# Kernel tuning notes

Hardware: AMD Instinct MI355X
Metric: run time of the kernel (lower is better)

Reference implementation:

```python
import jax, jax.numpy as jnp
import numpy as np

DIM = 2048
NUM_HEADS = 16
HEAD_DIM = DIM // NUM_HEADS
ROPE_BASE = 10000.0


def _rope_cos_sin(seq_len, head_dim, dtype):
    # lucidrains-style interleaved rotary embedding
    inv_freq = 1.0 / (ROPE_BASE ** (jnp.arange(0, head_dim, 2, dtype=jnp.float32) / head_dim))
    t = jnp.arange(seq_len, dtype=jnp.float32)
    freqs = t[:, None] * inv_freq[None, :]            # [n, d/2]
    freqs = jnp.repeat(freqs, 2, axis=-1)             # [n, d] interleaved repeat
    return jnp.cos(freqs).astype(dtype), jnp.sin(freqs).astype(dtype)


def _rotate_half(x):
    # interleaved pairs: (x1, x2) -> (-x2, x1)
    x = x.reshape(x.shape[:-1] + (x.shape[-1] // 2, 2))
    x1, x2 = x[..., 0], x[..., 1]
    return jnp.stack((-x2, x1), axis=-1).reshape(x.shape[:-2] + (-1,))


def _apply_rope(x, cos, sin):
    # x: [b, h, n, d]; cos/sin: [n, d]
    return x * cos + _rotate_half(x) * sin


def setup_inputs() -> dict:
    key = jax.random.key(0)
    ks = jax.random.split(key, 9)
    s = 1.0 / np.sqrt(DIM)
    x = jax.random.normal(ks[0], (2, 2048, DIM), dtype=jnp.float32)
    Wq = jax.random.normal(ks[1], (DIM, DIM), dtype=jnp.float32) * s
    Wk = jax.random.normal(ks[2], (DIM, DIM), dtype=jnp.float32) * s
    Wv = jax.random.normal(ks[3], (DIM, DIM), dtype=jnp.float32) * s
    Wo = jax.random.normal(ks[4], (DIM, DIM), dtype=jnp.float32) * s
    bq = jax.random.normal(ks[5], (DIM,), dtype=jnp.float32) * 0.01
    bk = jax.random.normal(ks[6], (DIM,), dtype=jnp.float32) * 0.01
    bv = jax.random.normal(ks[7], (DIM,), dtype=jnp.float32) * 0.01
    bo = jax.random.normal(ks[8], (DIM,), dtype=jnp.float32) * 0.01
    return {"x": x, "Wq": Wq, "bq": bq, "Wk": Wk, "bk": bk,
            "Wv": Wv, "bv": bv, "Wo": Wo, "bo": bo}


def reference(x, Wq, bq, Wk, bk, Wv, bv, Wo, bo):
    b, n, _ = x.shape
    h, d = NUM_HEADS, HEAD_DIM
    # Q/K/V projections; weights stored as [in, out]
    q = (x @ Wq + bq).reshape(b, n, h, d).transpose(0, 2, 1, 3)  # [b,h,n,d]
    k = (x @ Wk + bk).reshape(b, n, h, d).transpose(0, 2, 1, 3)
    v = (x @ Wv + bv).reshape(b, n, h, d).transpose(0, 2, 1, 3)
    cos, sin = _rope_cos_sin(n, d, x.dtype)
    q = _apply_rope(q, cos, sin)
    k = _apply_rope(k, cos, sin)
    # module divides q by sqrt(d), then SDPA applies its own 1/sqrt(d)
    scale = 1.0 / jnp.sqrt(jnp.asarray(d, dtype=x.dtype))
    q = q * scale
    logits = jnp.einsum('bhqd,bhkd->bhqk', q, k) * scale
    attn = jax.nn.softmax(logits, axis=-1)
    out = jnp.einsum('bhqk,bhkd->bhqd', attn, v)          # [b,h,n,d]
    out = out.transpose(0, 2, 1, 3).reshape(b, n, h * d)  # [b,n,dim]
    return out @ Wo + bo
```

## Files before the change

kernel.cpp:

```cpp
#include <hip/hip_runtime.h>
#include <hip/hip_bf16.h>
#include <math.h>

typedef unsigned short u16;
typedef unsigned int u32;
typedef __attribute__((ext_vector_type(8))) short short8;
typedef __attribute__((ext_vector_type(4))) float f32x4;

typedef const __attribute__((address_space(1))) u32 gu32;
typedef __attribute__((address_space(3))) u32 lu32;

#define DIM 2048
#define SEQ 2048
#define NH 16
#define HD 128

static __device__ __forceinline__ u16 f2b(float f) {
  __hip_bfloat16 h = __float2bfloat16(f);
  return __builtin_bit_cast(u16, h);
}
static __device__ __forceinline__ float b2f(u16 u) {
  __hip_bfloat16 h = __builtin_bit_cast(__hip_bfloat16, u);
  return __bfloat162float(h);
}

static __device__ __forceinline__ void g2l16(const u16* g, u16* l) {
  __builtin_amdgcn_global_load_lds((gu32*)g, (lu32*)l, 16, 0, 0);
}

__global__ __launch_bounds__(256) void prep_kernel(const float* __restrict__ x,
                                                   const float* __restrict__ Wq,
                                                   const float* __restrict__ Wk,
                                                   const float* __restrict__ Wv,
                                                   const float* __restrict__ Wo,
                                                   u16* __restrict__ xb,
                                                   u16* __restrict__ WT,
                                                   float* __restrict__ tab) {
  __shared__ float tile[64][65];
  int bid = blockIdx.x;
  int t = threadIdx.x;
  if (bid < 4096) {
    size_t i = ((size_t)bid * 256 + t) * 8;
    float4 a = *(const float4*)(x + i);
    float4 b = *(const float4*)(x + i + 4);
    uint4 o;
    o.x = (u32)f2b(a.x) | ((u32)f2b(a.y) << 16);
    o.y = (u32)f2b(a.z) | ((u32)f2b(a.w) << 16);
    o.z = (u32)f2b(b.x) | ((u32)f2b(b.y) << 16);
    o.w = (u32)f2b(b.z) | ((u32)f2b(b.w) << 16);
    *(uint4*)(xb + i) = o;
  } else if (bid < 8192) {
    int b2 = bid - 4096;
    int z = b2 >> 10;
    int rem = b2 & 1023;
    int by = rem >> 5, bx = rem & 31;
    const float* W = (z == 0) ? Wq : (z == 1) ? Wk : (z == 2) ? Wv : Wo;
    u16* dst = WT + (size_t)z * DIM * DIM;
    int k0 = by * 64, n0 = bx * 64;
    int c = (t & 15) * 4;
    int r = t >> 4;
#pragma unroll
    for (int i = 0; i < 4; ++i) {
      float4 v = *(const float4*)(W + (size_t)(k0 + r + 16 * i) * DIM + n0 + c);
      tile[r + 16 * i][c + 0] = v.x;
      tile[r + 16 * i][c + 1] = v.y;
      tile[r + 16 * i][c + 2] = v.z;
      tile[r + 16 * i][c + 3] = v.w;
    }
    __syncthreads();
#pragma unroll
    for (int i = 0; i < 4; ++i) {
      int rn = r + 16 * i;
      uint2 o;
      o.x = (u32)f2b(tile[c + 0][rn]) | ((u32)f2b(tile[c + 1][rn]) << 16);
      o.y = (u32)f2b(tile[c + 2][rn]) | ((u32)f2b(tile[c + 3][rn]) << 16);
      *(uint2*)(dst + (size_t)(n0 + rn) * DIM + k0 + c) = o;
    }
  } else {
    int idx = (bid - 8192) * 256 + t;
    int n = idx >> 6, j = idx & 63;
    double ang = (double)n * pow(10000.0, -(double)j / 64.0);
    tab[2 * idx + 0] = (float)cos(ang);
    tab[2 * idx + 1] = (float)sin(ang);
  }
}

__global__ __launch_bounds__(256, 2) void qkv_gemm_kernel(const u16* __restrict__ A,
                                                          const u16* __restrict__ Bt,
                                                          const float* __restrict__ bq,
                                                          const float* __restrict__ bk,
                                                          const float* __restrict__ bv,
                                                          const float* __restrict__ tab,
                                                          u16* __restrict__ Qbuf,
                                                          u16* __restrict__ Kbuf,
                                                          u16* __restrict__ Vtbf) {
  __shared__ u16 Asub[2][128 * 64];
  __shared__ u16 Bsub[2][128 * 64];
  int t = threadIdx.x;
  int lane = t & 63, wid = t >> 6;
  int L15 = lane & 15, quad = lane >> 4;
  int wm = (wid >> 1) * 64, wn = (wid & 1) * 64;
  int m0 = blockIdx.y * 128, n0 = blockIdx.x * 128;
  int srow = lane >> 3, schunk = lane & 7;

  f32x4 acc[4][4];
#pragma unroll
  for (int mi = 0; mi < 4; ++mi)
#pragma unroll
    for (int ni = 0; ni < 4; ++ni)
#pragma unroll
      for (int r = 0; r < 4; ++r) acc[mi][ni][r] = 0.f;

  auto stage = [&](int buf, int k0) {
#pragma unroll
    for (int i = 0; i < 4; ++i) {
      int ra = wid * 32 + i * 8 + srow;
      int cs = schunk ^ (ra & 7);
      g2l16(A + (size_t)(m0 + ra) * DIM + k0 + cs * 8, &Asub[buf][(wid * 32 + i * 8) * 64]);
      g2l16(Bt + (size_t)(n0 + ra) * DIM + k0 + cs * 8, &Bsub[buf][(wid * 32 + i * 8) * 64]);
    }
  };

  stage(0, 0);
  for (int it = 0; it < DIM / 64; ++it) {
    __syncthreads();
    if (it + 1 < DIM / 64) stage((it + 1) & 1, (it + 1) * 64);
    int buf = it & 1;
#pragma unroll
    for (int kc = 0; kc < 2; ++kc) {
      short8 af[4], bfr[4];
#pragma unroll
      for (int mi = 0; mi < 4; ++mi) {
        int row = wm + mi * 16 + L15;
        af[mi] = *(const short8*)(&Asub[buf][row * 64 + (((kc * 4 + quad) ^ (L15 & 7)) * 8)]);
      }
#pragma unroll
      for (int ni = 0; ni < 4; ++ni) {
        int row = wn + ni * 16 + L15;
        bfr[ni] = *(const short8*)(&Bsub[buf][row * 64 + (((kc * 4 + quad) ^ (L15 & 7)) * 8)]);
      }
#pragma unroll
      for (int mi = 0; mi < 4; ++mi)
#pragma unroll
        for (int ni = 0; ni < 4; ++ni)
          acc[mi][ni] = __builtin_amdgcn_mfma_f32_16x16x32_bf16(af[mi], bfr[ni], acc[mi][ni], 0, 0, 0);
    }
  }

  int which = n0 >> 11;
  const float* bp = (which == 0) ? bq : (which == 1) ? bk : bv;
#pragma unroll
  for (int mi = 0; mi < 4; ++mi) {
#pragma unroll
    for (int ni = 0; ni < 4; ++ni) {
      int colg = n0 + wn + ni * 16 + L15;
      int col = colg & 2047;
      float bvv = bp[col];
      int h = col >> 7, d = col & 127;
#pragma unroll
      for (int r = 0; r < 4; ++r) {
        int row = m0 + wm + mi * 16 + quad * 4 + r;
        int b = row >> 11, nseq = row & 2047;
        float v = acc[mi][ni][r] + bvv;
        if (which < 2) {
          int j = d >> 1;
          float2 cs = ((const float2*)tab)[nseq * 64 + j];
          float p = __shfl_xor(v, 1, 64);
          float o = (d & 1) ? (v * cs.x + p * cs.y) : (v * cs.x - p * cs.y);
          if (which == 0) o *= (1.0f / 128.0f);
          u16* dst = (which == 0) ? Qbuf : Kbuf;
          dst[((size_t)(b * 16 + h) * SEQ + nseq) * HD + d] = f2b(o);
        } else {
          Vtbf[((size_t)(b * 16 + h) * HD + d) * SEQ + nseq] = f2b(v);
        }
      }
    }
  }
}

__global__ __launch_bounds__(256, 2) void o_gemm_kernel(const u16* __restrict__ A,
                                                        const u16* __restrict__ Bt,
                                                        const float* __restrict__ bias,
                                                        float* __restrict__ Cout) {
  __shared__ u16 Asub[2][128 * 64];
  __shared__ u16 Bsub[2][128 * 64];
  int t = threadIdx.x;
  int lane = t & 63, wid = t >> 6;
  int L15 = lane & 15, quad = lane >> 4;
  int wm = (wid >> 1) * 64, wn = (wid & 1) * 64;
  int m0 = blockIdx.y * 128, n0 = blockIdx.x * 128;
  int srow = lane >> 3, schunk = lane & 7;

  f32x4 acc[4][4];
#pragma unroll
  for (int mi = 0; mi < 4; ++mi)
#pragma unroll
    for (int ni = 0; ni < 4; ++ni)
#pragma unroll
      for (int r = 0; r < 4; ++r) acc[mi][ni][r] = 0.f;

  auto stage = [&](int buf, int k0) {
#pragma unroll
    for (int i = 0; i < 4; ++i) {
      int ra = wid * 32 + i * 8 + srow;
      int cs = schunk ^ (ra & 7);
      g2l16(A + (size_t)(m0 + ra) * DIM + k0 + cs * 8, &Asub[buf][(wid * 32 + i * 8) * 64]);
      g2l16(Bt + (size_t)(n0 + ra) * DIM + k0 + cs * 8, &Bsub[buf][(wid * 32 + i * 8) * 64]);
    }
  };

  stage(0, 0);
  for (int it = 0; it < DIM / 64; ++it) {
    __syncthreads();
    if (it + 1 < DIM / 64) stage((it + 1) & 1, (it + 1) * 64);
    int buf = it & 1;
#pragma unroll
    for (int kc = 0; kc < 2; ++kc) {
      short8 af[4], bfr[4];
#pragma unroll
      for (int mi = 0; mi < 4; ++mi) {
        int row = wm + mi * 16 + L15;
        af[mi] = *(const short8*)(&Asub[buf][row * 64 + (((kc * 4 + quad) ^ (L15 & 7)) * 8)]);
      }
#pragma unroll
      for (int ni = 0; ni < 4; ++ni) {
        int row = wn + ni * 16 + L15;
        bfr[ni] = *(const short8*)(&Bsub[buf][row * 64 + (((kc * 4 + quad) ^ (L15 & 7)) * 8)]);
      }
#pragma unroll
      for (int mi = 0; mi < 4; ++mi)
#pragma unroll
        for (int ni = 0; ni < 4; ++ni)
          acc[mi][ni] = __builtin_amdgcn_mfma_f32_16x16x32_bf16(af[mi], bfr[ni], acc[mi][ni], 0, 0, 0);
    }
  }

#pragma unroll
  for (int mi = 0; mi < 4; ++mi) {
#pragma unroll
    for (int ni = 0; ni < 4; ++ni) {
      int col = n0 + wn + ni * 16 + L15;
      float bvv = bias[col];
#pragma unroll
      for (int r = 0; r < 4; ++r) {
        int row = m0 + wm + mi * 16 + quad * 4 + r;
        Cout[(size_t)row * DIM + col] = acc[mi][ni][r] + bvv;
      }
    }
  }
}

__global__ __launch_bounds__(512, 4) void attn_kernel(const u16* __restrict__ Q,
                                                      const u16* __restrict__ K,
                                                      const u16* __restrict__ Vt,
                                                      u16* __restrict__ ctx) {
  __shared__ u16 Ksub[2][64 * 128];
  __shared__ u16 Vsub[2][128 * 64];
  __shared__ u16 Psub[8][16 * 64];
  int t = threadIdx.x;
  int lane = t & 63, wid = t >> 6;
  int L15 = lane & 15, quad = lane >> 4;
  int bh = blockIdx.y;
  int q0 = blockIdx.x * 128 + wid * 16;

  short8 qf[4];
  const u16* Qb = Q + ((size_t)bh * SEQ + q0) * HD;
#pragma unroll
  for (int kc = 0; kc < 4; ++kc)
    qf[kc] = *(const short8*)(Qb + (size_t)L15 * HD + kc * 32 + quad * 8);

  float lsum[4];
  f32x4 oacc[8];
#pragma unroll
  for (int r = 0; r < 4; ++r) lsum[r] = 0.f;
#pragma unroll
  for (int nt = 0; nt < 8; ++nt)
#pragma unroll
    for (int r = 0; r < 4; ++r) oacc[nt][r] = 0.f;

  const u16* Kb = K + (size_t)bh * SEQ * HD;
  const u16* Vb = Vt + (size_t)bh * HD * SEQ;
  u16* Pw = &Psub[wid][0];

  int rkl = lane >> 4, ckl = lane & 15;
  int rvl = lane >> 3, cvl = lane & 7;

  auto stage = [&](int buf, int kt) {
#pragma unroll
    for (int i = 0; i < 2; ++i) {
      int j = wid + i * 8;
      int rk = j * 4 + rkl;
      int ck = ckl ^ (rk & 15);
      g2l16(Kb + (size_t)(kt + rk) * HD + ck * 8, &Ksub[buf][j * 4 * 128]);
      int rv = j * 8 + rvl;
      int cv = cvl ^ (rv & 7);
      g2l16(Vb + (size_t)rv * SEQ + kt + cv * 8, &Vsub[buf][j * 8 * 64]);
    }
  };

  stage(0, 0);
  for (int it = 0; it < SEQ / 64; ++it) {
    __syncthreads();
    if (it + 1 < SEQ / 64) stage((it + 1) & 1, (it + 1) * 64);
    int buf = it & 1;

    f32x4 sacc[4];
#pragma unroll
    for (int nt = 0; nt < 4; ++nt)
#pragma unroll
      for (int r = 0; r < 4; ++r) sacc[nt][r] = 0.f;
#pragma unroll
    for (int nt = 0; nt < 4; ++nt)
#pragma unroll
      for (int kc = 0; kc < 4; ++kc) {
        int row = nt * 16 + L15;
        short8 kf = *(const short8*)(&Ksub[buf][row * 128 + (((kc * 4 + quad) ^ L15) * 8)]);
        sacc[nt] = __builtin_amdgcn_mfma_f32_16x16x32_bf16(qf[kc], kf, sacc[nt], 0, 0, 0);
      }

#pragma unroll
    for (int nt = 0; nt < 4; ++nt)
#pragma unroll
      for (int r = 0; r < 4; ++r) {
        float e = __expf(sacc[nt][r]);
        lsum[r] += e;
        int row = quad * 4 + r;
        int col = nt * 16 + L15;
        int ch = (col >> 3) ^ (row & 7);
        Pw[row * 64 + ch * 8 + (col & 7)] = f2b(e);
      }

#pragma unroll
    for (int kc = 0; kc < 2; ++kc) {
      short8 pf = *(const short8*)(Pw + L15 * 64 + (((kc * 4 + quad) ^ (L15 & 7)) * 8));
#pragma unroll
      for (int nt = 0; nt < 8; ++nt) {
        int row = nt * 16 + L15;
        short8 vf = *(const short8*)(&Vsub[buf][row * 64 + (((kc * 4 + quad) ^ (L15 & 7)) * 8)]);
        oacc[nt] = __builtin_amdgcn_mfma_f32_16x16x32_bf16(pf, vf, oacc[nt], 0, 0, 0);
      }
    }
  }

#pragma unroll
  for (int off = 1; off < 16; off <<= 1)
#pragma unroll
    for (int r = 0; r < 4; ++r) lsum[r] += __shfl_xor(lsum[r], off, 64);

  int b = bh >> 4, h = bh & 15;
#pragma unroll
  for (int nt = 0; nt < 8; ++nt) {
    int d = nt * 16 + L15;
#pragma unroll
    for (int r = 0; r < 4; ++r) {
      int qrow = q0 + quad * 4 + r;
      float v = oacc[nt][r] / lsum[r];
      ctx[((size_t)b * SEQ + qrow) * DIM + h * HD + d] = f2b(v);
    }
  }
}

extern "C" void kernel_launch(void* const* d_in, const int* in_sizes, int n_in,
                              void* d_out, int out_size, void* d_ws, size_t ws_size,
                              hipStream_t stream) {
  (void)in_sizes; (void)n_in; (void)out_size; (void)ws_size;
  const float* x  = (const float*)d_in[0];
  const float* Wq = (const float*)d_in[1];
  const float* bq = (const float*)d_in[2];
  const float* Wk = (const float*)d_in[3];
  const float* bk = (const float*)d_in[4];
  const float* Wv = (const float*)d_in[5];
  const float* bv = (const float*)d_in[6];
  const float* Wo = (const float*)d_in[7];
  const float* bo = (const float*)d_in[8];

  u16* xb   = (u16*)d_ws;
  u16* WT   = xb   + (size_t)8388608;
  u16* Qbuf = WT   + (size_t)4 * 4194304;
  u16* Kbuf = Qbuf + (size_t)8388608;
  u16* Vtbf = Kbuf + (size_t)8388608;
  u16* ctx  = Vtbf + (size_t)8388608;
  float* tab = (float*)(ctx + (size_t)8388608);

  prep_kernel<<<8704, 256, 0, stream>>>(x, Wq, Wk, Wv, Wo, xb, WT, tab);
  qkv_gemm_kernel<<<dim3(48, 32), 256, 0, stream>>>(xb, WT, bq, bk, bv, tab,
                                                    Qbuf, Kbuf, Vtbf);
  attn_kernel<<<dim3(16, 32), 512, 0, stream>>>(Qbuf, Kbuf, Vtbf, ctx);
  o_gemm_kernel<<<dim3(16, 32), 256, 0, stream>>>(ctx, WT + (size_t)3 * 4194304, bo,
                                                  (float*)d_out);
}
```

Measured before the change: 434.3 us.

## Use 32x32 MFMA in GEMMs, software-pipeline QK in attention, remap blocks

Both projection GEMMs move from 16x16x32 to 32x32x16 bf16 MFMA with 2x2 accumulator tiles per wave. They also drop the LDS double buffer for a single-buffer load-sync-compute loop and remove the occupancy hint from launch bounds. The attention kernel now computes the next tile's QK^T scores before the PV matmul of the current tile, with separate K and V staging offsets, and uses a 1D grid remapped so groups of 8 heads share a query tile. The aim is fewer LDS reads per MFMA and better overlap of score computation with memory traffic. The cost is that the GEMMs lose overlap between global loads and math, and register pressure rises.

```diff
diff --git a/kernel.cpp b/kernel.cpp
--- a/kernel.cpp
+++ b/kernel.cpp
@@ -6,6 +6,7 @@
 typedef unsigned int u32;
 typedef __attribute__((ext_vector_type(8))) short short8;
 typedef __attribute__((ext_vector_type(4))) float f32x4;
+typedef __attribute__((ext_vector_type(16))) float f32x16;
 
 typedef const __attribute__((address_space(1))) u32 gu32;
 typedef __attribute__((address_space(3))) u32 lu32;
@@ -18,10 +19,6 @@
 static __device__ __forceinline__ u16 f2b(float f) {
   __hip_bfloat16 h = __float2bfloat16(f);
   return __builtin_bit_cast(u16, h);
-}
-static __device__ __forceinline__ float b2f(u16 u) {
-  __hip_bfloat16 h = __builtin_bit_cast(__hip_bfloat16, u);
-  return __bfloat162float(h);
 }
 
 static __device__ __forceinline__ void g2l16(const u16* g, u16* l) {
@@ -85,85 +82,72 @@
   }
 }
 
-__global__ __launch_bounds__(256, 2) void qkv_gemm_kernel(const u16* __restrict__ A,
-                                                          const u16* __restrict__ Bt,
-                                                          const float* __restrict__ bq,
-                                                          const float* __restrict__ bk,
-                                                          const float* __restrict__ bv,
-                                                          const float* __restrict__ tab,
-                                                          u16* __restrict__ Qbuf,
-                                                          u16* __restrict__ Kbuf,
-                                                          u16* __restrict__ Vtbf) {
-  __shared__ u16 Asub[2][128 * 64];
-  __shared__ u16 Bsub[2][128 * 64];
+__global__ __launch_bounds__(256) void qkv_gemm_kernel(const u16* __restrict__ A,
+                                                       const u16* __restrict__ Bt,
+                                                       const float* __restrict__ bq,
+                                                       const float* __restrict__ bk,
+                                                       const float* __restrict__ bv,
+                                                       const float* __restrict__ tab,
+                                                       u16* __restrict__ Qbuf,
+                                                       u16* __restrict__ Kbuf,
+                                                       u16* __restrict__ Vtbf) {
+  __shared__ u16 Asub[128 * 64];
+  __shared__ u16 Bsub[128 * 64];
   int t = threadIdx.x;
   int lane = t & 63, wid = t >> 6;
-  int L15 = lane & 15, quad = lane >> 4;
+  int L31 = lane & 31, half = lane >> 5;
   int wm = (wid >> 1) * 64, wn = (wid & 1) * 64;
   int m0 = blockIdx.y * 128, n0 = blockIdx.x * 128;
   int srow = lane >> 3, schunk = lane & 7;
 
-  f32x4 acc[4][4];
-#pragma unroll
-  for (int mi = 0; mi < 4; ++mi)
-#pragma unroll
-    for (int ni = 0; ni < 4; ++ni)
-#pragma unroll
-      for (int r = 0; r < 4; ++r) acc[mi][ni][r] = 0.f;
-
-  auto stage = [&](int buf, int k0) {
+  f32x16 acc[2][2];
+#pragma unroll
+  for (int mi = 0; mi < 2; ++mi)
+#pragma unroll
+    for (int ni = 0; ni < 2; ++ni)
+#pragma unroll
+      for (int r = 0; r < 16; ++r) acc[mi][ni][r] = 0.f;
+
+  for (int k0 = 0; k0 < DIM; k0 += 64) {
+    __syncthreads();
 #pragma unroll
     for (int i = 0; i < 4; ++i) {
       int ra = wid * 32 + i * 8 + srow;
       int cs = schunk ^ (ra & 7);
-      g2l16(A + (size_t)(m0 + ra) * DIM + k0 + cs * 8, &Asub[buf][(wid * 32 + i * 8) * 64]);
-      g2l16(Bt + (size_t)(n0 + ra) * DIM + k0 + cs * 8, &Bsub[buf][(wid * 32 + i * 8) * 64]);
-    }
-  };
-
-  stage(0, 0);
-  for (int it = 0; it < DIM / 64; ++it) {
-    __syncthreads();
-    if (it + 1 < DIM / 64) stage((it + 1) & 1, (it + 1) * 64);
-    int buf = it & 1;
-#pragma unroll
-    for (int kc = 0; kc < 2; ++kc) {
-      short8 af[4], bfr[4];
-#pragma unroll
-      for (int mi = 0; mi < 4; ++mi) {
-        int row = wm + mi * 16 + L15;
-        af[mi] = *(const short8*)(&Asub[buf][row * 64 + (((kc * 4 + quad) ^ (L15 & 7)) * 8)]);
-      }
-#pragma unroll
-      for (int ni = 0; ni < 4; ++ni) {
-        int row = wn + ni * 16 + L15;
-        bfr[ni] = *(const short8*)(&Bsub[buf][row * 64 + (((kc * 4 + quad) ^ (L15 & 7)) * 8)]);
-      }
-#pragma unroll
-      for (int mi = 0; mi < 4; ++mi)
-#pragma unroll
-        for (int ni = 0; ni < 4; ++ni)
-          acc[mi][ni] = __builtin_amdgcn_mfma_f32_16x16x32_bf16(af[mi], bfr[ni], acc[mi][ni], 0, 0, 0);
+      g2l16(A + (size_t)(m0 + ra) * DIM + k0 + cs * 8, Asub + (wid * 32 + i * 8) * 64);
+      g2l16(Bt + (size_t)(n0 + ra) * DIM + k0 + cs * 8, Bsub + (wid * 32 + i * 8) * 64);
+    }
+    __syncthreads();
+#pragma unroll
+    for (int ks = 0; ks < 4; ++ks) {
+      int co = (((ks * 2 + half) ^ (L31 & 7)) * 8);
+      short8 a0 = *(const short8*)(Asub + (wm + L31) * 64 + co);
+      short8 a1 = *(const short8*)(Asub + (wm + 32 + L31) * 64 + co);
+      short8 b0 = *(const short8*)(Bsub + (wn + L31) * 64 + co);
+      short8 b1 = *(const short8*)(Bsub + (wn + 32 + L31) * 64 + co);
+      acc[0][0] = __builtin_amdgcn_mfma_f32_32x32x16_bf16(a0, b0, acc[0][0], 0, 0, 0);
+      acc[0][1] = __builtin_amdgcn_mfma_f32_32x32x16_bf16(a0, b1, acc[0][1], 0, 0, 0);
+      acc[1][0] = __builtin_amdgcn_mfma_f32_32x32x16_bf16(a1, b0, acc[1][0], 0, 0, 0);
+      acc[1][1] = __builtin_amdgcn_mfma_f32_32x32x16_bf16(a1, b1, acc[1][1], 0, 0, 0);
     }
   }
 
   int which = n0 >> 11;
   const float* bp = (which == 0) ? bq : (which == 1) ? bk : bv;
 #pragma unroll
-  for (int mi = 0; mi < 4; ++mi) {
-#pragma unroll
-    for (int ni = 0; ni < 4; ++ni) {
-      int colg = n0 + wn + ni * 16 + L15;
+  for (int mi = 0; mi < 2; ++mi) {
+#pragma unroll
+    for (int ni = 0; ni < 2; ++ni) {
+      int colg = n0 + wn + ni * 32 + L31;
       int col = colg & 2047;
       float bvv = bp[col];
-      int h = col >> 7, d = col & 127;
-#pragma unroll
-      for (int r = 0; r < 4; ++r) {
-        int row = m0 + wm + mi * 16 + quad * 4 + r;
+      int h = col >> 7, d = col & 127, j = d >> 1;
+#pragma unroll
+      for (int r = 0; r < 16; ++r) {
+        int row = m0 + wm + mi * 32 + (r & 3) + 8 * (r >> 2) + 4 * half;
         int b = row >> 11, nseq = row & 2047;
         float v = acc[mi][ni][r] + bvv;
         if (which < 2) {
-          int j = d >> 1;
           float2 cs = ((const float2*)tab)[nseq * 64 + j];
           float p = __shfl_xor(v, 1, 64);
           float o = (d & 1) ? (v * cs.x + p * cs.y) : (v * cs.x - p * cs.y);
@@ -178,72 +162,60 @@
   }
 }
 
-__global__ __launch_bounds__(256, 2) void o_gemm_kernel(const u16* __restrict__ A,
-                                                        const u16* __restrict__ Bt,
-                                                        const float* __restrict__ bias,
-                                                        float* __restrict__ Cout) {
-  __shared__ u16 Asub[2][128 * 64];
-  __shared__ u16 Bsub[2][128 * 64];
+__global__ __launch_bounds__(256) void o_gemm_kernel(const u16* __restrict__ A,
+                                                     const u16* __restrict__ Bt,
+                                                     const float* __restrict__ bias,
+                                                     float* __restrict__ Cout) {
+  __shared__ u16 Asub[128 * 64];
+  __shared__ u16 Bsub[128 * 64];
   int t = threadIdx.x;
   int lane = t & 63, wid = t >> 6;
-  int L15 = lane & 15, quad = lane >> 4;
+  int L31 = lane & 31, half = lane >> 5;
   int wm = (wid >> 1) * 64, wn = (wid & 1) * 64;
   int m0 = blockIdx.y * 128, n0 = blockIdx.x * 128;
   int srow = lane >> 3, schunk = lane & 7;
 
-  f32x4 acc[4][4];
-#pragma unroll
-  for (int mi = 0; mi < 4; ++mi)
-#pragma unroll
-    for (int ni = 0; ni < 4; ++ni)
-#pragma unroll
-      for (int r = 0; r < 4; ++r) acc[mi][ni][r] = 0.f;
-
-  auto stage = [&](int buf, int k0) {
+  f32x16 acc[2][2];
+#pragma unroll
+  for (int mi = 0; mi < 2; ++mi)
+#pragma unroll
+    for (int ni = 0; ni < 2; ++ni)
+#pragma unroll
+      for (int r = 0; r < 16; ++r) acc[mi][ni][r] = 0.f;
+
+  for (int k0 = 0; k0 < DIM; k0 += 64) {
+    __syncthreads();
 #pragma unroll
     for (int i = 0; i < 4; ++i) {
       int ra = wid * 32 + i * 8 + srow;
       int cs = schunk ^ (ra & 7);
-      g2l16(A + (size_t)(m0 + ra) * DIM + k0 + cs * 8, &Asub[buf][(wid * 32 + i * 8) * 64]);
-      g2l16(Bt + (size_t)(n0 + ra) * DIM + k0 + cs * 8, &Bsub[buf][(wid * 32 + i * 8) * 64]);
-    }
-  };
-
-  stage(0, 0);
-  for (int it = 0; it < DIM / 64; ++it) {
-    __syncthreads();
-    if (it + 1 < DIM / 64) stage((it + 1) & 1, (it + 1) * 64);
-    int buf = it & 1;
-#pragma unroll
-    for (int kc = 0; kc < 2; ++kc) {
-      short8 af[4], bfr[4];
-#pragma unroll
-      for (int mi = 0; mi < 4; ++mi) {
-        int row = wm + mi * 16 + L15;
-        af[mi] = *(const short8*)(&Asub[buf][row * 64 + (((kc * 4 + quad) ^ (L15 & 7)) * 8)]);
-      }
-#pragma unroll
-      for (int ni = 0; ni < 4; ++ni) {
-        int row = wn + ni * 16 + L15;
-        bfr[ni] = *(const short8*)(&Bsub[buf][row * 64 + (((kc * 4 + quad) ^ (L15 & 7)) * 8)]);
-      }
-#pragma unroll
-      for (int mi = 0; mi < 4; ++mi)
-#pragma unroll
-        for (int ni = 0; ni < 4; ++ni)
-          acc[mi][ni] = __builtin_amdgcn_mfma_f32_16x16x32_bf16(af[mi], bfr[ni], acc[mi][ni], 0, 0, 0);
-    }
-  }
-
-#pragma unroll
-  for (int mi = 0; mi < 4; ++mi) {
-#pragma unroll
-    for (int ni = 0; ni < 4; ++ni) {
-      int col = n0 + wn + ni * 16 + L15;
+      g2l16(A + (size_t)(m0 + ra) * DIM + k0 + cs * 8, Asub + (wid * 32 + i * 8) * 64);
+      g2l16(Bt + (size_t)(n0 + ra) * DIM + k0 + cs * 8, Bsub + (wid * 32 + i * 8) * 64);
+    }
+    __syncthreads();
+#pragma unroll
+    for (int ks = 0; ks < 4; ++ks) {
+      int co = (((ks * 2 + half) ^ (L31 & 7)) * 8);
+      short8 a0 = *(const short8*)(Asub + (wm + L31) * 64 + co);
+      short8 a1 = *(const short8*)(Asub + (wm + 32 + L31) * 64 + co);
+      short8 b0 = *(const short8*)(Bsub + (wn + L31) * 64 + co);
+      short8 b1 = *(const short8*)(Bsub + (wn + 32 + L31) * 64 + co);
+      acc[0][0] = __builtin_amdgcn_mfma_f32_32x32x16_bf16(a0, b0, acc[0][0], 0, 0, 0);
+      acc[0][1] = __builtin_amdgcn_mfma_f32_32x32x16_bf16(a0, b1, acc[0][1], 0, 0, 0);
+      acc[1][0] = __builtin_amdgcn_mfma_f32_32x32x16_bf16(a1, b0, acc[1][0], 0, 0, 0);
+      acc[1][1] = __builtin_amdgcn_mfma_f32_32x32x16_bf16(a1, b1, acc[1][1], 0, 0, 0);
+    }
+  }
+
+#pragma unroll
+  for (int mi = 0; mi < 2; ++mi) {
+#pragma unroll
+    for (int ni = 0; ni < 2; ++ni) {
+      int col = n0 + wn + ni * 32 + L31;
       float bvv = bias[col];
 #pragma unroll
-      for (int r = 0; r < 4; ++r) {
-        int row = m0 + wm + mi * 16 + quad * 4 + r;
+      for (int r = 0; r < 16; ++r) {
+        int row = m0 + wm + mi * 32 + (r & 3) + 8 * (r >> 2) + 4 * half;
         Cout[(size_t)row * DIM + col] = acc[mi][ni][r] + bvv;
       }
     }
@@ -260,8 +232,10 @@
   int t = threadIdx.x;
   int lane = t & 63, wid = t >> 6;
   int L15 = lane & 15, quad = lane >> 4;
-  int bh = blockIdx.y;
-  int q0 = blockIdx.x * 128 + wid * 16;
+  int lin = blockIdx.x;
+  int bh = (lin & 7) + ((lin >> 7) << 3);
+  int qt = (lin >> 3) & 15;
+  int q0 = qt * 128 + wid * 16;
 
   short8 qf[4];
   const u16* Qb = Q + ((size_t)bh * SEQ + q0) * HD;
@@ -285,38 +259,50 @@
   int rkl = lane >> 4, ckl = lane & 15;
   int rvl = lane >> 3, cvl = lane & 7;
 
-  auto stage = [&](int buf, int kt) {
+  auto stageK = [&](int buf, int kt) {
 #pragma unroll
     for (int i = 0; i < 2; ++i) {
       int j = wid + i * 8;
       int rk = j * 4 + rkl;
       int ck = ckl ^ (rk & 15);
       g2l16(Kb + (size_t)(kt + rk) * HD + ck * 8, &Ksub[buf][j * 4 * 128]);
+    }
+  };
+  auto stageV = [&](int buf, int kt) {
+#pragma unroll
+    for (int i = 0; i < 2; ++i) {
+      int j = wid + i * 8;
       int rv = j * 8 + rvl;
       int cv = cvl ^ (rv & 7);
       g2l16(Vb + (size_t)rv * SEQ + kt + cv * 8, &Vsub[buf][j * 8 * 64]);
     }
   };
-
-  stage(0, 0);
-  for (int it = 0; it < SEQ / 64; ++it) {
-    __syncthreads();
-    if (it + 1 < SEQ / 64) stage((it + 1) & 1, (it + 1) * 64);
-    int buf = it & 1;
-
-    f32x4 sacc[4];
-#pragma unroll
-    for (int nt = 0; nt < 4; ++nt)
-#pragma unroll
-      for (int r = 0; r < 4; ++r) sacc[nt][r] = 0.f;
-#pragma unroll
-    for (int nt = 0; nt < 4; ++nt)
+  auto computeS = [&](int buf, f32x4* s) {
+#pragma unroll
+    for (int nt = 0; nt < 4; ++nt) {
+#pragma unroll
+      for (int r = 0; r < 4; ++r) s[nt][r] = 0.f;
 #pragma unroll
       for (int kc = 0; kc < 4; ++kc) {
         int row = nt * 16 + L15;
         short8 kf = *(const short8*)(&Ksub[buf][row * 128 + (((kc * 4 + quad) ^ L15) * 8)]);
-        sacc[nt] = __builtin_amdgcn_mfma_f32_16x16x32_bf16(qf[kc], kf, sacc[nt], 0, 0, 0);
-      }
+        s[nt] = __builtin_amdgcn_mfma_f32_16x16x32_bf16(qf[kc], kf, s[nt], 0, 0, 0);
+      }
+    }
+  };
+
+  f32x4 sacc[4];
+  stageK(0, 0);
+  stageV(0, 0);
+  __syncthreads();
+  computeS(0, sacc);
+  stageK(1, 64);
+  __syncthreads();
+
+  for (int it = 0; it < SEQ / 64; ++it) {
+    int cb = it & 1, nb = cb ^ 1;
+    if (it + 2 < SEQ / 64) stageK(cb, (it + 2) * 64);
+    if (it + 1 < SEQ / 64) stageV(nb, (it + 1) * 64);
 
 #pragma unroll
     for (int nt = 0; nt < 4; ++nt)
@@ -330,16 +316,24 @@
         Pw[row * 64 + ch * 8 + (col & 7)] = f2b(e);
       }
 
+    f32x4 snew[4];
+    if (it + 1 < SEQ / 64) computeS(nb, snew);
+
 #pragma unroll
     for (int kc = 0; kc < 2; ++kc) {
       short8 pf = *(const short8*)(Pw + L15 * 64 + (((kc * 4 + quad) ^ (L15 & 7)) * 8));
 #pragma unroll
       for (int nt = 0; nt < 8; ++nt) {
         int row = nt * 16 + L15;
-        short8 vf = *(const short8*)(&Vsub[buf][row * 64 + (((kc * 4 + quad) ^ (L15 & 7)) * 8)]);
+        short8 vf = *(const short8*)(&Vsub[cb][row * 64 + (((kc * 4 + quad) ^ (L15 & 7)) * 8)]);
         oacc[nt] = __builtin_amdgcn_mfma_f32_16x16x32_bf16(pf, vf, oacc[nt], 0, 0, 0);
       }
     }
+    if (it + 1 < SEQ / 64) {
+#pragma unroll
+      for (int nt = 0; nt < 4; ++nt) sacc[nt] = snew[nt];
+    }
+    __syncthreads();
   }
 
 #pragma unroll
@@ -385,7 +379,7 @@
   prep_kernel<<<8704, 256, 0, stream>>>(x, Wq, Wk, Wv, Wo, xb, WT, tab);
   qkv_gemm_kernel<<<dim3(48, 32), 256, 0, stream>>>(xb, WT, bq, bk, bv, tab,
                                                     Qbuf, Kbuf, Vtbf);
-  attn_kernel<<<dim3(16, 32), 512, 0, stream>>>(Qbuf, Kbuf, Vtbf, ctx);
+  attn_kernel<<<512, 512, 0, stream>>>(Qbuf, Kbuf, Vtbf, ctx);
   o_gemm_kernel<<<dim3(16, 32), 256, 0, stream>>>(ctx, WT + (size_t)3 * 4194304, bo,
                                                   (float*)d_out);
 }
```

Measured after the change: 440.6 us. No clear change (+1.4%).

## Retile QKV GEMM to 256-row blocks, software-pipeline attention S/PV, remap attention grid

Applied to the files above, without the earlier changes.

The QKV GEMM now uses 512-thread blocks covering 256 rows with single-buffered LDS, and packs V-transpose stores into 32-bit writes. The attention kernel splits K and V staging and computes the next tile's QK^T scores while the current P·V runs, prefetching K two tiles ahead. It also remaps the attention grid to a 1D launch that groups 8 heads per q-tile for L2 locality. The aim is to overlap MFMA work with softmax and memory loads, but dropping the GEMM double buffer exposes load latency and the extra score accumulators raise register pressure.

```diff
diff --git a/kernel.cpp b/kernel.cpp
--- a/kernel.cpp
+++ b/kernel.cpp
@@ -18,10 +18,6 @@
 static __device__ __forceinline__ u16 f2b(float f) {
   __hip_bfloat16 h = __float2bfloat16(f);
   return __builtin_bit_cast(u16, h);
-}
-static __device__ __forceinline__ float b2f(u16 u) {
-  __hip_bfloat16 h = __builtin_bit_cast(__hip_bfloat16, u);
-  return __bfloat162float(h);
 }
 
 static __device__ __forceinline__ void g2l16(const u16* g, u16* l) {
@@ -85,7 +81,7 @@
   }
 }
 
-__global__ __launch_bounds__(256, 2) void qkv_gemm_kernel(const u16* __restrict__ A,
+__global__ __launch_bounds__(512, 4) void qkv_gemm_kernel(const u16* __restrict__ A,
                                                           const u16* __restrict__ Bt,
                                                           const float* __restrict__ bq,
                                                           const float* __restrict__ bk,
@@ -94,13 +90,13 @@
                                                           u16* __restrict__ Qbuf,
                                                           u16* __restrict__ Kbuf,
                                                           u16* __restrict__ Vtbf) {
-  __shared__ u16 Asub[2][128 * 64];
-  __shared__ u16 Bsub[2][128 * 64];
+  __shared__ u16 Asub[256 * 64];
+  __shared__ u16 Bsub[128 * 64];
   int t = threadIdx.x;
   int lane = t & 63, wid = t >> 6;
   int L15 = lane & 15, quad = lane >> 4;
   int wm = (wid >> 1) * 64, wn = (wid & 1) * 64;
-  int m0 = blockIdx.y * 128, n0 = blockIdx.x * 128;
+  int m0 = blockIdx.y * 256, n0 = blockIdx.x * 128;
   int srow = lane >> 3, schunk = lane & 7;
 
   f32x4 acc[4][4];
@@ -111,33 +107,35 @@
 #pragma unroll
       for (int r = 0; r < 4; ++r) acc[mi][ni][r] = 0.f;
 
-  auto stage = [&](int buf, int k0) {
+  for (int k0 = 0; k0 < DIM; k0 += 64) {
+    __syncthreads();
 #pragma unroll
     for (int i = 0; i < 4; ++i) {
-      int ra = wid * 32 + i * 8 + srow;
-      int cs = schunk ^ (ra & 7);
-      g2l16(A + (size_t)(m0 + ra) * DIM + k0 + cs * 8, &Asub[buf][(wid * 32 + i * 8) * 64]);
-      g2l16(Bt + (size_t)(n0 + ra) * DIM + k0 + cs * 8, &Bsub[buf][(wid * 32 + i * 8) * 64]);
-    }
-  };
-
-  stage(0, 0);
-  for (int it = 0; it < DIM / 64; ++it) {
+      int base = wid * 32 + i * 8;
+      int ra = base + srow;
+      int cs = schunk ^ (srow & 7);
+      g2l16(A + (size_t)(m0 + ra) * DIM + k0 + cs * 8, Asub + base * 64);
+    }
+#pragma unroll
+    for (int i = 0; i < 2; ++i) {
+      int base = wid * 16 + i * 8;
+      int rb = base + srow;
+      int cs = schunk ^ (srow & 7);
+      g2l16(Bt + (size_t)(n0 + rb) * DIM + k0 + cs * 8, Bsub + base * 64);
+    }
     __syncthreads();
-    if (it + 1 < DIM / 64) stage((it + 1) & 1, (it + 1) * 64);
-    int buf = it & 1;
 #pragma unroll
     for (int kc = 0; kc < 2; ++kc) {
       short8 af[4], bfr[4];
 #pragma unroll
       for (int mi = 0; mi < 4; ++mi) {
         int row = wm + mi * 16 + L15;
-        af[mi] = *(const short8*)(&Asub[buf][row * 64 + (((kc * 4 + quad) ^ (L15 & 7)) * 8)]);
+        af[mi] = *(const short8*)(Asub + row * 64 + (((kc * 4 + quad) ^ (L15 & 7)) * 8));
       }
 #pragma unroll
       for (int ni = 0; ni < 4; ++ni) {
         int row = wn + ni * 16 + L15;
-        bfr[ni] = *(const short8*)(&Bsub[buf][row * 64 + (((kc * 4 + quad) ^ (L15 & 7)) * 8)]);
+        bfr[ni] = *(const short8*)(Bsub + row * 64 + (((kc * 4 + quad) ^ (L15 & 7)) * 8));
       }
 #pragma unroll
       for (int mi = 0; mi < 4; ++mi)
@@ -157,21 +155,29 @@
       int col = colg & 2047;
       float bvv = bp[col];
       int h = col >> 7, d = col & 127;
-#pragma unroll
-      for (int r = 0; r < 4; ++r) {
-        int row = m0 + wm + mi * 16 + quad * 4 + r;
-        int b = row >> 11, nseq = row & 2047;
-        float v = acc[mi][ni][r] + bvv;
-        if (which < 2) {
-          int j = d >> 1;
+      if (which < 2) {
+        int j = d >> 1;
+#pragma unroll
+        for (int r = 0; r < 4; ++r) {
+          int row = m0 + wm + mi * 16 + quad * 4 + r;
+          int b = row >> 11, nseq = row & 2047;
+          float v = acc[mi][ni][r] + bvv;
           float2 cs = ((const float2*)tab)[nseq * 64 + j];
           float p = __shfl_xor(v, 1, 64);
           float o = (d & 1) ? (v * cs.x + p * cs.y) : (v * cs.x - p * cs.y);
           if (which == 0) o *= (1.0f / 128.0f);
           u16* dst = (which == 0) ? Qbuf : Kbuf;
           dst[((size_t)(b * 16 + h) * SEQ + nseq) * HD + d] = f2b(o);
-        } else {
-          Vtbf[((size_t)(b * 16 + h) * HD + d) * SEQ + nseq] = f2b(v);
+        }
+      } else {
+#pragma unroll
+        for (int rp = 0; rp < 2; ++rp) {
+          int row = m0 + wm + mi * 16 + quad * 4 + rp * 2;
+          int b = row >> 11, nseq = row & 2047;
+          float v0 = acc[mi][ni][rp * 2] + bvv;
+          float v1 = acc[mi][ni][rp * 2 + 1] + bvv;
+          u32 pk = (u32)f2b(v0) | ((u32)f2b(v1) << 16);
+          *(u32*)(Vtbf + ((size_t)(b * 16 + h) * HD + d) * SEQ + nseq) = pk;
         }
       }
     }
@@ -260,8 +266,10 @@
   int t = threadIdx.x;
   int lane = t & 63, wid = t >> 6;
   int L15 = lane & 15, quad = lane >> 4;
-  int bh = blockIdx.y;
-  int q0 = blockIdx.x * 128 + wid * 16;
+  int lin = blockIdx.x;
+  int bh = (lin & 7) + ((lin >> 7) << 3);
+  int qt = (lin >> 3) & 15;
+  int q0 = qt * 128 + wid * 16;
 
   short8 qf[4];
   const u16* Qb = Q + ((size_t)bh * SEQ + q0) * HD;
@@ -285,38 +293,50 @@
   int rkl = lane >> 4, ckl = lane & 15;
   int rvl = lane >> 3, cvl = lane & 7;
 
-  auto stage = [&](int buf, int kt) {
+  auto stageK = [&](int buf, int kt) {
 #pragma unroll
     for (int i = 0; i < 2; ++i) {
       int j = wid + i * 8;
       int rk = j * 4 + rkl;
       int ck = ckl ^ (rk & 15);
       g2l16(Kb + (size_t)(kt + rk) * HD + ck * 8, &Ksub[buf][j * 4 * 128]);
+    }
+  };
+  auto stageV = [&](int buf, int kt) {
+#pragma unroll
+    for (int i = 0; i < 2; ++i) {
+      int j = wid + i * 8;
       int rv = j * 8 + rvl;
       int cv = cvl ^ (rv & 7);
       g2l16(Vb + (size_t)rv * SEQ + kt + cv * 8, &Vsub[buf][j * 8 * 64]);
     }
   };
-
-  stage(0, 0);
-  for (int it = 0; it < SEQ / 64; ++it) {
-    __syncthreads();
-    if (it + 1 < SEQ / 64) stage((it + 1) & 1, (it + 1) * 64);
-    int buf = it & 1;
-
-    f32x4 sacc[4];
-#pragma unroll
-    for (int nt = 0; nt < 4; ++nt)
-#pragma unroll
-      for (int r = 0; r < 4; ++r) sacc[nt][r] = 0.f;
-#pragma unroll
-    for (int nt = 0; nt < 4; ++nt)
+  auto computeS = [&](int buf, f32x4* s) {
+#pragma unroll
+    for (int nt = 0; nt < 4; ++nt) {
+#pragma unroll
+      for (int r = 0; r < 4; ++r) s[nt][r] = 0.f;
 #pragma unroll
       for (int kc = 0; kc < 4; ++kc) {
         int row = nt * 16 + L15;
         short8 kf = *(const short8*)(&Ksub[buf][row * 128 + (((kc * 4 + quad) ^ L15) * 8)]);
-        sacc[nt] = __builtin_amdgcn_mfma_f32_16x16x32_bf16(qf[kc], kf, sacc[nt], 0, 0, 0);
-      }
+        s[nt] = __builtin_amdgcn_mfma_f32_16x16x32_bf16(qf[kc], kf, s[nt], 0, 0, 0);
+      }
+    }
+  };
+
+  f32x4 sacc[4];
+  stageK(0, 0);
+  stageV(0, 0);
+  __syncthreads();
+  computeS(0, sacc);
+  stageK(1, 64);
+  __syncthreads();
+
+  for (int it = 0; it < SEQ / 64; ++it) {
+    int cb = it & 1, nb = cb ^ 1;
+    if (it + 2 < SEQ / 64) stageK(cb, (it + 2) * 64);
+    if (it + 1 < SEQ / 64) stageV(nb, (it + 1) * 64);
 
 #pragma unroll
     for (int nt = 0; nt < 4; ++nt)
@@ -330,16 +350,24 @@
         Pw[row * 64 + ch * 8 + (col & 7)] = f2b(e);
       }
 
+    f32x4 snew[4];
+    if (it + 1 < SEQ / 64) computeS(nb, snew);
+
 #pragma unroll
     for (int kc = 0; kc < 2; ++kc) {
       short8 pf = *(const short8*)(Pw + L15 * 64 + (((kc * 4 + quad) ^ (L15 & 7)) * 8));
 #pragma unroll
       for (int nt = 0; nt < 8; ++nt) {
         int row = nt * 16 + L15;
-        short8 vf = *(const short8*)(&Vsub[buf][row * 64 + (((kc * 4 + quad) ^ (L15 & 7)) * 8)]);
+        short8 vf = *(const short8*)(&Vsub[cb][row * 64 + (((kc * 4 + quad) ^ (L15 & 7)) * 8)]);
         oacc[nt] = __builtin_amdgcn_mfma_f32_16x16x32_bf16(pf, vf, oacc[nt], 0, 0, 0);
       }
     }
+    if (it + 1 < SEQ / 64) {
+#pragma unroll
+      for (int nt = 0; nt < 4; ++nt) sacc[nt] = snew[nt];
+    }
+    __syncthreads();
   }
 
 #pragma unroll
@@ -383,9 +411,9 @@
   float* tab = (float*)(ctx + (size_t)8388608);
 
   prep_kernel<<<8704, 256, 0, stream>>>(x, Wq, Wk, Wv, Wo, xb, WT, tab);
-  qkv_gemm_kernel<<<dim3(48, 32), 256, 0, stream>>>(xb, WT, bq, bk, bv, tab,
+  qkv_gemm_kernel<<<dim3(48, 16), 512, 0, stream>>>(xb, WT, bq, bk, bv, tab,
                                                     Qbuf, Kbuf, Vtbf);
-  attn_kernel<<<dim3(16, 32), 512, 0, stream>>>(Qbuf, Kbuf, Vtbf, ctx);
+  attn_kernel<<<512, 512, 0, stream>>>(Qbuf, Kbuf, Vtbf, ctx);
   o_gemm_kernel<<<dim3(16, 32), 256, 0, stream>>>(ctx, WT + (size_t)3 * 4194304, bo,
                                                   (float*)d_out);
 }
```

Result: faster. 419.7 us (-3.4%).
